# Kernel optimization log

Measured on AMD Instinct MI355X. Metric: run time of the kernel, lower is better.

Reference implementation:

```python
import jax, jax.numpy as jnp
import numpy as np


def setup_inputs() -> dict:
    key = jax.random.key(0)
    k1, k2 = jax.random.split(key)
    B, H, W, D = 4096, 64, 64, 512
    inputs = jax.random.normal(k1, (B, D), dtype=jnp.float32)
    # keras 'random_uniform' initializer default range [-0.05, 0.05]
    weights_map = jax.random.uniform(k2, (H, W, D), dtype=jnp.float32,
                                     minval=-0.05, maxval=0.05)
    return {"inputs": inputs, "weights_map": weights_map}


def reference(inputs, weights_map):
    # inputs: (B, D); weights_map: (H, W, D)
    H, W, D = weights_map.shape
    flat_w = weights_map.reshape(-1, D)              # (N, D), N = H*W
    # avoids materializing the (B, N, D) difference tensor)
    x_sq = jnp.sum(inputs * inputs, axis=1, keepdims=True)    # (B, 1)
    w_sq = jnp.sum(flat_w * flat_w, axis=1)                   # (N,)
    sq_dist = x_sq - 2.0 * (inputs @ flat_w.T) + w_sq         # (B, N)
    sq_dist = jnp.maximum(sq_dist, 0.0)
    bmu_flat = jnp.argmin(sq_dist, axis=1)                    # (B,)
    bmu_y = (bmu_flat // W).astype(jnp.int32)
    bmu_x = (bmu_flat % W).astype(jnp.int32)
    bmu_indices = jnp.stack([bmu_y, bmu_x], axis=1)           # (B, 2)
    min_sq = jnp.take_along_axis(sq_dist, bmu_flat[:, None], axis=1)[:, 0]
    quantization_errors = jnp.sqrt(min_sq)                    # (B,)
    return bmu_indices, quantization_errors
```

## Files before the change

### kernel.cpp

```cpp
#include <hip/hip_runtime.h>

#define B_ROWS 4096
#define N_COLS 4096
#define DIM    512
#define LDK    1024

typedef __attribute__((ext_vector_type(8))) short short8;
typedef __attribute__((ext_vector_type(4))) float floatx4;

__device__ __forceinline__ unsigned short f2bf_rn(float f) {
    unsigned u = __float_as_uint(f);
    u += 0x7fffu + ((u >> 16) & 1u);
    return (unsigned short)(u >> 16);
}
__device__ __forceinline__ float bf2f(unsigned short h) {
    return __uint_as_float(((unsigned)h) << 16);
}

__device__ __forceinline__ unsigned long long pack_key(float v, int idx) {
    unsigned u = __float_as_uint(v);
    u = (u & 0x80000000u) ? ~u : (u | 0x80000000u);
    return ((unsigned long long)u << 32) | (unsigned)idx;
}

__device__ __forceinline__ void async16(const unsigned short* g, unsigned short* l) {
    __builtin_amdgcn_global_load_lds(
        (__attribute__((address_space(1))) void*)g,
        (__attribute__((address_space(3))) void*)l, 16, 0, 0);
}

__global__ __launch_bounds__(256) void som_convert(
    const float* __restrict__ X, const float* __restrict__ Wt,
    unsigned short* __restrict__ Xc, unsigned short* __restrict__ Wc,
    float* __restrict__ x_sq, float* __restrict__ w_sq,
    unsigned long long* __restrict__ packed)
{
    int wave = threadIdx.x >> 6, lane = threadIdx.x & 63;
    int grow = blockIdx.x * 4 + wave;
    bool isX = grow < B_ROWS;
    const float* src = isX ? (X + (size_t)grow * DIM)
                           : (Wt + (size_t)(grow - B_ROWS) * DIM);
    const float4* p4 = (const float4*)src;
    float4 a = p4[lane * 2], b = p4[lane * 2 + 1];
    float f[8] = {a.x, a.y, a.z, a.w, b.x, b.y, b.z, b.w};
    short8 hi, lo;
    float s = 0.f;
    #pragma unroll
    for (int t = 0; t < 8; ++t) {
        unsigned short h = f2bf_rn(f[t]);
        hi[t] = (short)h;
        lo[t] = (short)f2bf_rn(f[t] - bf2f(h));
        s = fmaf(f[t], f[t], s);
    }
    unsigned short* dst = (isX ? Xc + (size_t)grow * LDK
                               : Wc + (size_t)(grow - B_ROWS) * LDK) + lane * 8;
    *(short8*)(dst)       = hi;
    *(short8*)(dst + 512) = lo;
    #pragma unroll
    for (int off = 32; off >= 1; off >>= 1) s += __shfl_xor(s, off, 64);
    if (lane == 0) {
        if (isX) { x_sq[grow] = s; packed[grow] = ~0ull; }
        else     { w_sq[grow - B_ROWS] = s; }
    }
}

__global__ __launch_bounds__(256, 3) void som_dist_v7(
    const unsigned short* __restrict__ Xc, const unsigned short* __restrict__ Wc,
    const float* __restrict__ w_sq, unsigned long long* __restrict__ packed)
{
    __shared__ __align__(16) unsigned short Ah[128 * 32];
    __shared__ __align__(16) unsigned short Al[128 * 32];
    __shared__ __align__(16) unsigned short Bh[128 * 32];
    __shared__ __align__(16) unsigned short Bl[128 * 32];
    const int tid  = threadIdx.x;
    const int wave = tid >> 6, lane = tid & 63;
    const int wr = wave >> 1, wc = wave & 1;
    const int bm = blockIdx.y, bn = blockIdx.x;
    const int quad = lane >> 4, t16 = lane & 15;

    const int srow = lane >> 2;
    const int scol = ((((lane & 3) - ((lane >> 3) & 3)) & 3)) * 8;
    const unsigned short* gAh = Xc + (size_t)(bm * 128 + wave * 32 + srow) * LDK + scol;
    const unsigned short* gBh = Wc + (size_t)(bn * 128 + wave * 32 + srow) * LDK + scol;
    const unsigned short* gAl = gAh + 512;
    const unsigned short* gBl = gBh + 512;
    unsigned short* lAh = &Ah[(wave * 32) * 32];
    unsigned short* lAl = &Al[(wave * 32) * 32];
    unsigned short* lBh = &Bh[(wave * 32) * 32];
    unsigned short* lBl = &Bl[(wave * 32) * 32];

    const int rdw = 4 * t16 + ((quad + ((t16 >> 1) & 3)) & 3);
    const unsigned short* pah = &Ah[wr * 2048 + rdw * 8];
    const unsigned short* pal = &Al[wr * 2048 + rdw * 8];
    const unsigned short* pbh = &Bh[wc * 2048 + rdw * 8];
    const unsigned short* pbl = &Bl[wc * 2048 + rdw * 8];

    floatx4 acc[4][4];
    #pragma unroll
    for (int i = 0; i < 4; ++i)
        #pragma unroll
        for (int j = 0; j < 4; ++j) acc[i][j] = (floatx4){0.f, 0.f, 0.f, 0.f};

    #pragma unroll 1
    for (int k0 = 0; k0 < DIM; k0 += 32) {
        __syncthreads();
        async16(gAh + k0,            lAh);
        async16(gAh + k0 + 16 * LDK, lAh + 512);
        async16(gAl + k0,            lAl);
        async16(gAl + k0 + 16 * LDK, lAl + 512);
        async16(gBh + k0,            lBh);
        async16(gBh + k0 + 16 * LDK, lBh + 512);
        async16(gBl + k0,            lBl);
        async16(gBl + k0 + 16 * LDK, lBl + 512);
        __syncthreads();

        short8 ah[4], bh[4], x[4];
        #pragma unroll
        for (int i = 0; i < 4; ++i) ah[i] = *(const short8*)(pah + i * 512);
        #pragma unroll
        for (int j = 0; j < 4; ++j) bh[j] = *(const short8*)(pbh + j * 512);
        #pragma unroll
        for (int i = 0; i < 4; ++i)
            #pragma unroll
            for (int j = 0; j < 4; ++j)
                acc[i][j] = __builtin_amdgcn_mfma_f32_16x16x32_bf16(
                    ah[i], bh[j], acc[i][j], 0, 0, 0);

        #pragma unroll
        for (int j = 0; j < 4; ++j) x[j] = *(const short8*)(pbl + j * 512);
        #pragma unroll
        for (int i = 0; i < 4; ++i)
            #pragma unroll
            for (int j = 0; j < 4; ++j)
                acc[i][j] = __builtin_amdgcn_mfma_f32_16x16x32_bf16(
                    ah[i], x[j], acc[i][j], 0, 0, 0);

        #pragma unroll
        for (int i = 0; i < 4; ++i) x[i] = *(const short8*)(pal + i * 512);
        #pragma unroll
        for (int i = 0; i < 4; ++i)
            #pragma unroll
            for (int j = 0; j < 4; ++j)
                acc[i][j] = __builtin_amdgcn_mfma_f32_16x16x32_bf16(
                    x[i], bh[j], acc[i][j], 0, 0, 0);
    }

    const int col0 = bn * 128 + wc * 64 + t16;
    float wq[4];
    #pragma unroll
    for (int j = 0; j < 4; ++j) wq[j] = w_sq[col0 + j * 16];
    const int row_base = bm * 128 + wr * 64 + quad * 4;
    #pragma unroll
    for (int i = 0; i < 4; ++i) {
        #pragma unroll
        for (int r = 0; r < 4; ++r) {
            unsigned long long best = ~0ull;
            #pragma unroll
            for (int j = 0; j < 4; ++j) {
                float val = fmaf(-2.f, acc[i][j][r], wq[j]);
                unsigned long long key = pack_key(val, col0 + j * 16);
                best = (key < best) ? key : best;
            }
            #pragma unroll
            for (int m = 1; m <= 8; m <<= 1) {
                unsigned long long o = __shfl_xor(best, m, 64);
                best = (o < best) ? o : best;
            }
            if (t16 == 0)
                atomicMin(&packed[row_base + i * 16 + r], best);
        }
    }
}

__global__ __launch_bounds__(256) void som_finalize(
    const unsigned long long* __restrict__ packed,
    const float* __restrict__ x_sq, float* __restrict__ out)
{
    int b = blockIdx.x * 256 + threadIdx.x;
    unsigned long long p = packed[b];
    unsigned idx = (unsigned)(p & 0xffffffffull);
    unsigned key = (unsigned)(p >> 32);
    unsigned u = (key & 0x80000000u) ? (key & 0x7fffffffu) : ~key;
    float val = __uint_as_float(u);
    float sq = fmaxf(x_sq[b] + val, 0.f);
    out[2 * b]     = (float)(idx >> 6);
    out[2 * b + 1] = (float)(idx & 63);
    out[2 * B_ROWS + b] = sqrtf(sq);
}

extern "C" void kernel_launch(void* const* d_in, const int* in_sizes, int n_in,
                              void* d_out, int out_size, void* d_ws, size_t ws_size,
                              hipStream_t stream) {
    const float* X  = (const float*)d_in[0];
    const float* Wt = (const float*)d_in[1];
    float* out = (float*)d_out;

    unsigned long long* packed = (unsigned long long*)d_ws;
    float* x_sq = (float*)((char*)d_ws + (32 << 10));
    float* w_sq = (float*)((char*)d_ws + (48 << 10));
    unsigned short* Xc = (unsigned short*)((char*)d_ws + (64 << 10));
    unsigned short* Wc = (unsigned short*)((char*)d_ws + (64 << 10) + ((size_t)B_ROWS * LDK * 2));

    som_convert<<<dim3((B_ROWS + N_COLS) / 4), dim3(256), 0, stream>>>(
        X, Wt, Xc, Wc, x_sq, w_sq, packed);
    som_dist_v7<<<dim3(N_COLS / 128, B_ROWS / 128), dim3(256), 0, stream>>>(
        Xc, Wc, w_sq, packed);
    som_finalize<<<dim3(B_ROWS / 256), dim3(256), 0, stream>>>(packed, x_sq, out);
}
```

Measured before the change: 124.0 us.

## Double-buffer LDS tiles with async prefetch two K-steps ahead

Replaces the single-buffered LDS tiles with two 32 KB buffers and prefetches the K-slice two steps ahead using global_load_lds. Explicit vmcnt waits and s_barrier replace the two __syncthreads per iteration, so the next tile's loads overlap the MFMA work. Wave priority is raised around the MFMA bursts. The cost is double the LDS per block, which lowers the occupancy target from 3 to 2 blocks, and the correctness of the hand-written waitcnt logic becomes harder to verify.

```diff
diff --git a/kernel.cpp b/kernel.cpp
--- a/kernel.cpp
+++ b/kernel.cpp
@@ -64,14 +64,11 @@
     }
 }
 
-__global__ __launch_bounds__(256, 3) void som_dist_v7(
+__global__ __launch_bounds__(256, 2) void som_dist_v8(
     const unsigned short* __restrict__ Xc, const unsigned short* __restrict__ Wc,
     const float* __restrict__ w_sq, unsigned long long* __restrict__ packed)
 {
-    __shared__ __align__(16) unsigned short Ah[128 * 32];
-    __shared__ __align__(16) unsigned short Al[128 * 32];
-    __shared__ __align__(16) unsigned short Bh[128 * 32];
-    __shared__ __align__(16) unsigned short Bl[128 * 32];
+    __shared__ __align__(16) unsigned short L[2 * 16384];
     const int tid  = threadIdx.x;
     const int wave = tid >> 6, lane = tid & 63;
     const int wr = wave >> 1, wc = wave & 1;
@@ -84,16 +81,11 @@
     const unsigned short* gBh = Wc + (size_t)(bn * 128 + wave * 32 + srow) * LDK + scol;
     const unsigned short* gAl = gAh + 512;
     const unsigned short* gBl = gBh + 512;
-    unsigned short* lAh = &Ah[(wave * 32) * 32];
-    unsigned short* lAl = &Al[(wave * 32) * 32];
-    unsigned short* lBh = &Bh[(wave * 32) * 32];
-    unsigned short* lBl = &Bl[(wave * 32) * 32];
+    const int wofs = wave * 1024;
 
     const int rdw = 4 * t16 + ((quad + ((t16 >> 1) & 3)) & 3);
-    const unsigned short* pah = &Ah[wr * 2048 + rdw * 8];
-    const unsigned short* pal = &Al[wr * 2048 + rdw * 8];
-    const unsigned short* pbh = &Bh[wc * 2048 + rdw * 8];
-    const unsigned short* pbl = &Bl[wc * 2048 + rdw * 8];
+    const int ra = wr * 2048 + rdw * 8;
+    const int rb = 8192 + wc * 2048 + rdw * 8;
 
     floatx4 acc[4][4];
     #pragma unroll
@@ -101,48 +93,78 @@
         #pragma unroll
         for (int j = 0; j < 4; ++j) acc[i][j] = (floatx4){0.f, 0.f, 0.f, 0.f};
 
+    #pragma unroll
+    for (int b = 0; b < 2; ++b) {
+        unsigned short* base = &L[b * 16384];
+        const int k0 = b * 32;
+        async16(gAh + k0,            base + wofs);
+        async16(gAh + k0 + 16 * LDK, base + wofs + 512);
+        async16(gAl + k0,            base + 4096 + wofs);
+        async16(gAl + k0 + 16 * LDK, base + 4096 + wofs + 512);
+        async16(gBh + k0,            base + 8192 + wofs);
+        async16(gBh + k0 + 16 * LDK, base + 8192 + wofs + 512);
+        async16(gBl + k0,            base + 12288 + wofs);
+        async16(gBl + k0 + 16 * LDK, base + 12288 + wofs + 512);
+    }
+
     #pragma unroll 1
-    for (int k0 = 0; k0 < DIM; k0 += 32) {
-        __syncthreads();
-        async16(gAh + k0,            lAh);
-        async16(gAh + k0 + 16 * LDK, lAh + 512);
-        async16(gAl + k0,            lAl);
-        async16(gAl + k0 + 16 * LDK, lAl + 512);
-        async16(gBh + k0,            lBh);
-        async16(gBh + k0 + 16 * LDK, lBh + 512);
-        async16(gBl + k0,            lBl);
-        async16(gBl + k0 + 16 * LDK, lBl + 512);
-        __syncthreads();
-
-        short8 ah[4], bh[4], x[4];
-        #pragma unroll
-        for (int i = 0; i < 4; ++i) ah[i] = *(const short8*)(pah + i * 512);
-        #pragma unroll
-        for (int j = 0; j < 4; ++j) bh[j] = *(const short8*)(pbh + j * 512);
+    for (int kt = 0; kt < 16; ++kt) {
+        const int cur = kt & 1;
+        unsigned short* base = &L[cur * 16384];
+
+        if (kt == 15) asm volatile("s_waitcnt vmcnt(0)" ::: "memory");
+        else          asm volatile("s_waitcnt vmcnt(8)" ::: "memory");
+        __builtin_amdgcn_s_barrier();
+
+        short8 ah[4], bh[4], bl[4], al[4];
+        #pragma unroll
+        for (int i = 0; i < 4; ++i) ah[i] = *(const short8*)(base + ra + i * 512);
+        #pragma unroll
+        for (int j = 0; j < 4; ++j) bh[j] = *(const short8*)(base + rb + j * 512);
+
+        __builtin_amdgcn_s_setprio(1);
         #pragma unroll
         for (int i = 0; i < 4; ++i)
             #pragma unroll
             for (int j = 0; j < 4; ++j)
                 acc[i][j] = __builtin_amdgcn_mfma_f32_16x16x32_bf16(
                     ah[i], bh[j], acc[i][j], 0, 0, 0);
-
-        #pragma unroll
-        for (int j = 0; j < 4; ++j) x[j] = *(const short8*)(pbl + j * 512);
+        __builtin_amdgcn_s_setprio(0);
+
+        #pragma unroll
+        for (int j = 0; j < 4; ++j) bl[j] = *(const short8*)(base + rb + 4096 + j * 512);
+        #pragma unroll
+        for (int i = 0; i < 4; ++i) al[i] = *(const short8*)(base + ra + 4096 + i * 512);
+
+        asm volatile("s_waitcnt lgkmcnt(0)" ::: "memory");
+        __builtin_amdgcn_s_barrier();
+
+        if (kt < 14) {
+            const int k0 = (kt + 2) * 32;
+            async16(gAh + k0,            base + wofs);
+            async16(gAh + k0 + 16 * LDK, base + wofs + 512);
+            async16(gAl + k0,            base + 4096 + wofs);
+            async16(gAl + k0 + 16 * LDK, base + 4096 + wofs + 512);
+            async16(gBh + k0,            base + 8192 + wofs);
+            async16(gBh + k0 + 16 * LDK, base + 8192 + wofs + 512);
+            async16(gBl + k0,            base + 12288 + wofs);
+            async16(gBl + k0 + 16 * LDK, base + 12288 + wofs + 512);
+        }
+
+        __builtin_amdgcn_s_setprio(1);
         #pragma unroll
         for (int i = 0; i < 4; ++i)
             #pragma unroll
             for (int j = 0; j < 4; ++j)
                 acc[i][j] = __builtin_amdgcn_mfma_f32_16x16x32_bf16(
-                    ah[i], x[j], acc[i][j], 0, 0, 0);
-
-        #pragma unroll
-        for (int i = 0; i < 4; ++i) x[i] = *(const short8*)(pal + i * 512);
+                    ah[i], bl[j], acc[i][j], 0, 0, 0);
         #pragma unroll
         for (int i = 0; i < 4; ++i)
             #pragma unroll
             for (int j = 0; j < 4; ++j)
                 acc[i][j] = __builtin_amdgcn_mfma_f32_16x16x32_bf16(
-                    x[i], bh[j], acc[i][j], 0, 0, 0);
+                    al[i], bh[j], acc[i][j], 0, 0, 0);
+        __builtin_amdgcn_s_setprio(0);
     }
 
     const int col0 = bn * 128 + wc * 64 + t16;
@@ -203,7 +225,7 @@
 
     som_convert<<<dim3((B_ROWS + N_COLS) / 4), dim3(256), 0, stream>>>(
         X, Wt, Xc, Wc, x_sq, w_sq, packed);
-    som_dist_v7<<<dim3(N_COLS / 128, B_ROWS / 128), dim3(256), 0, stream>>>(
+    som_dist_v8<<<dim3(N_COLS / 128, B_ROWS / 128), dim3(256), 0, stream>>>(
         Xc, Wc, w_sq, packed);
     som_finalize<<<dim3(B_ROWS / 256), dim3(256), 0, stream>>>(packed, x_sq, out);
 }
```

New measurement: 127.5 us. 1.03x slower.
